# Kernel tuning notes

Measured on AMD Instinct MI355X. Metric: run time of the kernel, lower is better.

## Reference

```python
import jax, jax.numpy as jnp
import numpy as np


def _pairwise_sq_dists(p, t):
    # p: [N,3], t: [M,3] -> [N,M] squared euclidean distances
    # |p|^2 + |t|^2 - 2 p.t^T (avoids materializing [N,M,3])
    p2 = jnp.sum(p * p, axis=-1)  # [N]
    t2 = jnp.sum(t * t, axis=-1)  # [M]
    cross = jnp.einsum('nd,md->nm', p, t)  # [N,M]
    d = p2[:, None] + t2[None, :] - 2.0 * cross
    return jnp.maximum(d, 0.0)  # clamp tiny negatives from cancellation


def setup_inputs() -> dict:
    key = jax.random.key(0)
    k1, k2 = jax.random.split(key)
    N = 16384
    predict = jax.random.normal(k1, (1, N, 3), dtype=jnp.float32)
    target = jax.random.normal(k2, (1, N, 3), dtype=jnp.float32)
    return {"predict": predict, "target": target}


def reference(predict, target):
    # Faithful to forward: only the first batch element is used.
    p = predict[0]  # [N,3]
    t = target[0]   # [M,3]
    d = _pairwise_sq_dists(p, t)          # [N,M] squared distances
    dist1 = jnp.min(d, axis=1)            # nearest target for each predict pt
    dist2 = jnp.min(d, axis=0)            # nearest predict for each target pt
    loss = jnp.mean(dist1) + jnp.mean(dist2)
    return loss
```

## Files before the change

kernel.cpp:

```cpp
#include <hip/hip_runtime.h>


typedef short s16x8 __attribute__((ext_vector_type(8)));
typedef float f32x16 __attribute__((ext_vector_type(16)));

static __device__ __forceinline__ unsigned short f2bf(float f) {
    unsigned u = __float_as_uint(f);
    unsigned r = (u + 0x7FFFu + ((u >> 16) & 1u)) >> 16;
    return (unsigned short)r;
}
static __device__ __forceinline__ float bf2f(unsigned short h) {
    return __uint_as_float(((unsigned)h) << 16);
}
static __device__ __forceinline__ void split2(float v, unsigned short& h, unsigned short& l) {
    h = f2bf(v);
    l = f2bf(v - bf2f(h));
}

union Pack16 { unsigned short u[16]; uint4 v[2]; };

__global__ void prep_pack(const float* __restrict__ predict, const float* __restrict__ target,
                          unsigned short* __restrict__ ApP, unsigned short* __restrict__ BpP,
                          unsigned short* __restrict__ ApT, unsigned short* __restrict__ BpT,
                          int N)
{
    int i = blockIdx.x * blockDim.x + threadIdx.x;
    if (i >= 2 * N) return;
    const float* src = (i < N) ? predict : target;
    unsigned short* Ap = (i < N) ? ApP : ApT;
    unsigned short* Bp = (i < N) ? BpP : BpT;
    int j = (i < N) ? i : i - N;

    float x = src[3*j], y = src[3*j+1], z = src[3*j+2];
    float n2 = __builtin_fmaf(x, x, __builtin_fmaf(y, y, z*z));

    unsigned short xh,xl,yh,yl,zh,zl,nh,nl,qxh,qxl,qyh,qyl,qzh,qzl;
    split2(x, xh, xl); split2(y, yh, yl); split2(z, zh, zl); split2(n2, nh, nl);
    split2(-2.0f*x, qxh, qxl); split2(-2.0f*y, qyh, qyl); split2(-2.0f*z, qzh, qzl);
    const unsigned short one = f2bf(1.0f);

    Pack16 a, b;
    a.u[0]=xh; a.u[1]=xh; a.u[2]=xl; a.u[3]=xl;
    a.u[4]=yh; a.u[5]=yh; a.u[6]=yl; a.u[7]=yl;
    a.u[8]=zh; a.u[9]=zh; a.u[10]=zl; a.u[11]=zl;
    a.u[12]=nh; a.u[13]=nl; a.u[14]=one; a.u[15]=one;

    b.u[0]=qxh; b.u[1]=qxl; b.u[2]=qxh; b.u[3]=qxl;
    b.u[4]=qyh; b.u[5]=qyl; b.u[6]=qyh; b.u[7]=qyl;
    b.u[8]=qzh; b.u[9]=qzl; b.u[10]=qzh; b.u[11]=qzl;
    b.u[12]=one; b.u[13]=one; b.u[14]=nh; b.u[15]=nl;

    uint4* ad = (uint4*)(Ap + (size_t)j * 16);
    uint4* bd = (uint4*)(Bp + (size_t)j * 16);
    ad[0] = a.v[0]; ad[1] = a.v[1];
    bd[0] = b.v[0]; bd[1] = b.v[1];
}

#define TB 64

__global__ __launch_bounds__(256, 2) void chamfer_main(
    const unsigned short* __restrict__ ApP, const unsigned short* __restrict__ BpP,
    const unsigned short* __restrict__ ApT, const unsigned short* __restrict__ BpT,
    float* __restrict__ partials, int N)
{
    const int dir = blockIdx.z;
    const unsigned short* __restrict__ Ap = dir ? ApT : ApP;
    const unsigned short* __restrict__ Bp = dir ? BpP : BpT;
    float* __restrict__ pout = partials + (size_t)(dir * 4 + blockIdx.y) * N;

    __shared__ unsigned short lB[TB * 32 * 16];

    const int tid  = threadIdx.x;
    const int w    = tid >> 6;
    const int lane = tid & 63;
    const int lm   = lane & 31;
    const int lg   = lane >> 5;

    const int row0 = blockIdx.x * 256 + w * 64;

    const uint4* A4 = (const uint4*)Ap;
    s16x8 a0 = __builtin_bit_cast(s16x8, A4[(size_t)(row0      + lm) * 2 + lg]);
    s16x8 a1 = __builtin_bit_cast(s16x8, A4[(size_t)(row0 + 32 + lm) * 2 + lg]);

    float rm0[16], rm1[16];
    #pragma unroll
    for (int r = 0; r < 16; ++r) { rm0[r] = 3.0e38f; rm1[r] = 3.0e38f; }

    const f32x16 zc = {0.f,0.f,0.f,0.f,0.f,0.f,0.f,0.f,0.f,0.f,0.f,0.f,0.f,0.f,0.f,0.f};

    const uint4* gB = (const uint4*)(Bp + (size_t)blockIdx.y * (N / 4) * 16);
    uint4* lds4 = (uint4*)lB;
    const int nchunk = (N / 4) / (TB * 32);

    for (int chunk = 0; chunk < nchunk; ++chunk) {
        __syncthreads();
        const uint4* gsrc = gB + (size_t)chunk * (TB * 32 * 2);
        #pragma unroll
        for (int it = 0; it < (TB * 32 * 2) / 256; ++it)
            lds4[it * 256 + tid] = gsrc[it * 256 + tid];
        __syncthreads();

        #pragma unroll 2
        for (int t = 0; t < TB; ++t) {
            uint4 bv = *(const uint4*)(lB + t * 512 + lm * 16 + lg * 8);
            s16x8 b = __builtin_bit_cast(s16x8, bv);
            f32x16 acc0 = __builtin_amdgcn_mfma_f32_32x32x16_bf16(a0, b, zc, 0, 0, 0);
            f32x16 acc1 = __builtin_amdgcn_mfma_f32_32x32x16_bf16(a1, b, zc, 0, 0, 0);
            #pragma unroll
            for (int r = 0; r < 16; ++r) {
                rm0[r] = fminf(rm0[r], acc0[r]);
                rm1[r] = fminf(rm1[r], acc1[r]);
            }
        }
    }

    #pragma unroll
    for (int m = 1; m <= 16; m <<= 1) {
        #pragma unroll
        for (int r = 0; r < 16; ++r) {
            rm0[r] = fminf(rm0[r], __shfl_xor(rm0[r], m, 64));
            rm1[r] = fminf(rm1[r], __shfl_xor(rm1[r], m, 64));
        }
    }
    #pragma unroll
    for (int r = 0; r < 16; ++r) {
        int rl = (r & 3) + 8 * (r >> 2) + 4 * lg;
        if (lm == r) {
            pout[row0 +      rl] = rm0[r];
            pout[row0 + 32 + rl] = rm1[r];
        }
    }
}

__global__ void chamfer_reduce(const float* __restrict__ partials, float* __restrict__ out, int N) {
    __shared__ double sacc[16];
    const int tid = threadIdx.x;
    double acc = 0.0;
    for (int i = tid; i < N; i += blockDim.x) {
        float m0 = fminf(fminf(partials[i],         partials[N + i]),
                         fminf(partials[2*N + i],   partials[3*N + i]));
        float m1 = fminf(fminf(partials[4*N + i],   partials[5*N + i]),
                         fminf(partials[6*N + i],   partials[7*N + i]));
        acc += (double)fmaxf(m0, 0.0f) + (double)fmaxf(m1, 0.0f);
    }
    for (int off = 32; off; off >>= 1)
        acc += __shfl_down(acc, off, 64);
    const int wave = tid >> 6, lane = tid & 63;
    if (lane == 0) sacc[wave] = acc;
    __syncthreads();
    if (tid == 0) {
        double t = 0.0;
        int nw = blockDim.x >> 6;
        for (int wv = 0; wv < nw; ++wv) t += sacc[wv];
        out[0] = (float)(t / (double)N);
    }
}

extern "C" void kernel_launch(void* const* d_in, const int* in_sizes, int n_in,
                              void* d_out, int out_size, void* d_ws, size_t ws_size,
                              hipStream_t stream) {
    const float* predict = (const float*)d_in[0];
    const float* target  = (const float*)d_in[1];
    const int N = in_sizes[0] / 3;

    unsigned short* ws16 = (unsigned short*)d_ws;
    unsigned short* ApP = ws16;
    unsigned short* BpP = ws16 + (size_t)1 * N * 16;
    unsigned short* ApT = ws16 + (size_t)2 * N * 16;
    unsigned short* BpT = ws16 + (size_t)3 * N * 16;
    float* partials = (float*)(ws16 + (size_t)4 * N * 16);

    prep_pack<<<dim3((2 * N + 255) / 256), dim3(256), 0, stream>>>(
        predict, target, ApP, BpP, ApT, BpT, N);

    dim3 grid(N / 256, 4, 2);
    chamfer_main<<<grid, dim3(256), 0, stream>>>(ApP, BpP, ApT, BpT, partials, N);

    chamfer_reduce<<<1, dim3(1024), 0, stream>>>(partials, (float*)d_out, N);
}
```

Before: 85.67 us.

## Read B operands directly from global with register prefetch, split columns 8 ways, parallelize reduction

The main kernel stops staging B tiles through LDS with barriers. Each lane now loads its B fragment straight from global or L2 memory, prefetching the next pair one iteration ahead, and issues four MFMAs per step. The column dimension is split 8 ways instead of 4, which doubles the grid and the partials buffer. The final reduction becomes a 16-block vectorized pass followed by a tiny finishing kernel, at the cost of one more launch and more global traffic from each wave, since B is no longer shared through LDS.

```diff
diff --git a/kernel.cpp b/kernel.cpp
--- a/kernel.cpp
+++ b/kernel.cpp
@@ -56,7 +56,7 @@
     bd[0] = b.v[0]; bd[1] = b.v[1];
 }
 
-#define TB 64
+#define CG 8
 
 __global__ __launch_bounds__(256, 2) void chamfer_main(
     const unsigned short* __restrict__ ApP, const unsigned short* __restrict__ BpP,
@@ -66,9 +66,7 @@
     const int dir = blockIdx.z;
     const unsigned short* __restrict__ Ap = dir ? ApT : ApP;
     const unsigned short* __restrict__ Bp = dir ? BpP : BpT;
-    float* __restrict__ pout = partials + (size_t)(dir * 4 + blockIdx.y) * N;
-
-    __shared__ unsigned short lB[TB * 32 * 16];
+    float* __restrict__ pout = partials + (size_t)(dir * CG + blockIdx.y) * N;
 
     const int tid  = threadIdx.x;
     const int w    = tid >> 6;
@@ -88,29 +86,42 @@
 
     const f32x16 zc = {0.f,0.f,0.f,0.f,0.f,0.f,0.f,0.f,0.f,0.f,0.f,0.f,0.f,0.f,0.f,0.f};
 
-    const uint4* gB = (const uint4*)(Bp + (size_t)blockIdx.y * (N / 4) * 16);
-    uint4* lds4 = (uint4*)lB;
-    const int nchunk = (N / 4) / (TB * 32);
-
-    for (int chunk = 0; chunk < nchunk; ++chunk) {
-        __syncthreads();
-        const uint4* gsrc = gB + (size_t)chunk * (TB * 32 * 2);
-        #pragma unroll
-        for (int it = 0; it < (TB * 32 * 2) / 256; ++it)
-            lds4[it * 256 + tid] = gsrc[it * 256 + tid];
-        __syncthreads();
-
-        #pragma unroll 2
-        for (int t = 0; t < TB; ++t) {
-            uint4 bv = *(const uint4*)(lB + t * 512 + lm * 16 + lg * 8);
-            s16x8 b = __builtin_bit_cast(s16x8, bv);
-            f32x16 acc0 = __builtin_amdgcn_mfma_f32_32x32x16_bf16(a0, b, zc, 0, 0, 0);
-            f32x16 acc1 = __builtin_amdgcn_mfma_f32_32x32x16_bf16(a1, b, zc, 0, 0, 0);
-            #pragma unroll
-            for (int r = 0; r < 16; ++r) {
-                rm0[r] = fminf(rm0[r], acc0[r]);
-                rm1[r] = fminf(rm1[r], acc1[r]);
-            }
+    const int npt = N / CG;
+    const int NT  = npt / 32;
+    const uint4* bp = (const uint4*)Bp + (size_t)blockIdx.y * npt * 2 + lm * 2 + lg;
+
+    uint4 c0 = bp[0];
+    uint4 c1 = bp[64];
+    const uint4* bnext = bp + 128;
+
+    for (int t = 0; t < NT - 2; t += 2) {
+        uint4 n0 = bnext[0];
+        uint4 n1 = bnext[64];
+        bnext += 128;
+        s16x8 bA = __builtin_bit_cast(s16x8, c0);
+        s16x8 bB = __builtin_bit_cast(s16x8, c1);
+        f32x16 p0 = __builtin_amdgcn_mfma_f32_32x32x16_bf16(a0, bA, zc, 0, 0, 0);
+        f32x16 q0 = __builtin_amdgcn_mfma_f32_32x32x16_bf16(a0, bB, zc, 0, 0, 0);
+        f32x16 p1 = __builtin_amdgcn_mfma_f32_32x32x16_bf16(a1, bA, zc, 0, 0, 0);
+        f32x16 q1 = __builtin_amdgcn_mfma_f32_32x32x16_bf16(a1, bB, zc, 0, 0, 0);
+        #pragma unroll
+        for (int r = 0; r < 16; ++r) {
+            rm0[r] = fminf(fminf(rm0[r], p0[r]), q0[r]);
+            rm1[r] = fminf(fminf(rm1[r], p1[r]), q1[r]);
+        }
+        c0 = n0; c1 = n1;
+    }
+    {
+        s16x8 bA = __builtin_bit_cast(s16x8, c0);
+        s16x8 bB = __builtin_bit_cast(s16x8, c1);
+        f32x16 p0 = __builtin_amdgcn_mfma_f32_32x32x16_bf16(a0, bA, zc, 0, 0, 0);
+        f32x16 q0 = __builtin_amdgcn_mfma_f32_32x32x16_bf16(a0, bB, zc, 0, 0, 0);
+        f32x16 p1 = __builtin_amdgcn_mfma_f32_32x32x16_bf16(a1, bA, zc, 0, 0, 0);
+        f32x16 q1 = __builtin_amdgcn_mfma_f32_32x32x16_bf16(a1, bB, zc, 0, 0, 0);
+        #pragma unroll
+        for (int r = 0; r < 16; ++r) {
+            rm0[r] = fminf(fminf(rm0[r], p0[r]), q0[r]);
+            rm1[r] = fminf(fminf(rm1[r], p1[r]), q1[r]);
         }
     }
 
@@ -132,26 +143,49 @@
     }
 }
 
-__global__ void chamfer_reduce(const float* __restrict__ partials, float* __restrict__ out, int N) {
-    __shared__ double sacc[16];
-    const int tid = threadIdx.x;
+__global__ void chamfer_reduce1(const float* __restrict__ partials,
+                                double* __restrict__ bsum, int N)
+{
+    const int n4 = N >> 2;
+    const float4* p4 = (const float4*)partials;
     double acc = 0.0;
-    for (int i = tid; i < N; i += blockDim.x) {
-        float m0 = fminf(fminf(partials[i],         partials[N + i]),
-                         fminf(partials[2*N + i],   partials[3*N + i]));
-        float m1 = fminf(fminf(partials[4*N + i],   partials[5*N + i]),
-                         fminf(partials[6*N + i],   partials[7*N + i]));
-        acc += (double)fmaxf(m0, 0.0f) + (double)fmaxf(m1, 0.0f);
+    for (int i = blockIdx.x * blockDim.x + threadIdx.x; i < n4;
+         i += gridDim.x * blockDim.x) {
+        float4 m0 = p4[i];
+        #pragma unroll
+        for (int g = 1; g < CG; ++g) {
+            float4 v = p4[(size_t)g * n4 + i];
+            m0.x = fminf(m0.x, v.x); m0.y = fminf(m0.y, v.y);
+            m0.z = fminf(m0.z, v.z); m0.w = fminf(m0.w, v.w);
+        }
+        float4 m1 = p4[(size_t)CG * n4 + i];
+        #pragma unroll
+        for (int g = CG + 1; g < 2 * CG; ++g) {
+            float4 v = p4[(size_t)g * n4 + i];
+            m1.x = fminf(m1.x, v.x); m1.y = fminf(m1.y, v.y);
+            m1.z = fminf(m1.z, v.z); m1.w = fminf(m1.w, v.w);
+        }
+        acc += (double)fmaxf(m0.x, 0.0f) + (double)fmaxf(m0.y, 0.0f)
+             + (double)fmaxf(m0.z, 0.0f) + (double)fmaxf(m0.w, 0.0f)
+             + (double)fmaxf(m1.x, 0.0f) + (double)fmaxf(m1.y, 0.0f)
+             + (double)fmaxf(m1.z, 0.0f) + (double)fmaxf(m1.w, 0.0f);
     }
     for (int off = 32; off; off >>= 1)
         acc += __shfl_down(acc, off, 64);
-    const int wave = tid >> 6, lane = tid & 63;
+    __shared__ double sacc[4];
+    const int wave = threadIdx.x >> 6, lane = threadIdx.x & 63;
     if (lane == 0) sacc[wave] = acc;
     __syncthreads();
-    if (tid == 0) {
+    if (threadIdx.x == 0)
+        bsum[blockIdx.x] = sacc[0] + sacc[1] + sacc[2] + sacc[3];
+}
+
+__global__ void chamfer_reduce2(const double* __restrict__ bsum,
+                                float* __restrict__ out, int N, int nb)
+{
+    if (threadIdx.x == 0) {
         double t = 0.0;
-        int nw = blockDim.x >> 6;
-        for (int wv = 0; wv < nw; ++wv) t += sacc[wv];
+        for (int i = 0; i < nb; ++i) t += bsum[i];
         out[0] = (float)(t / (double)N);
     }
 }
@@ -169,12 +203,14 @@
     unsigned short* ApT = ws16 + (size_t)2 * N * 16;
     unsigned short* BpT = ws16 + (size_t)3 * N * 16;
     float* partials = (float*)(ws16 + (size_t)4 * N * 16);
+    double* bsum = (double*)(partials + (size_t)2 * CG * N);
 
     prep_pack<<<dim3((2 * N + 255) / 256), dim3(256), 0, stream>>>(
         predict, target, ApP, BpP, ApT, BpT, N);
 
-    dim3 grid(N / 256, 4, 2);
+    dim3 grid(N / 256, CG, 2);
     chamfer_main<<<grid, dim3(256), 0, stream>>>(ApP, BpP, ApT, BpT, partials, N);
 
-    chamfer_reduce<<<1, dim3(1024), 0, stream>>>(partials, (float*)d_out, N);
-}
+    chamfer_reduce1<<<dim3(16), dim3(256), 0, stream>>>(partials, bsum, N);
+    chamfer_reduce2<<<dim3(1), dim3(64), 0, stream>>>(bsum, (float*)d_out, N, 16);
+}
```

Measured after the change: 83.60 us. 2.4% less time.
